# Kernel tuning notes

Measured on AMD Instinct MI355X. Metric: run time of the kernel, lower is better.

Reference implementation:

```python
import jax, jax.numpy as jnp
import numpy as np

UNITS = 4096        # output channels
IN_DIM = 4096       # row_count
LEVELS = 16         # codebook entries per output channel (4-bit)
GROUP = 128         # group_size
NGROUPS = (IN_DIM + GROUP - 1) // GROUP  # 32
BATCH = 16


def setup_inputs() -> dict:
    key = jax.random.key(0)
    k1, k2, k3, k4, k5, k6 = jax.random.split(key, 6)
    inputs = jax.random.normal(k1, (BATCH, IN_DIM), dtype=jnp.float32)
    codebooks = jax.random.normal(k2, (UNITS, LEVELS), dtype=jnp.float32)
    scales = jax.random.uniform(k3, (UNITS, NGROUPS), dtype=jnp.float32)
    residual = jax.random.normal(k4, (UNITS, NGROUPS, GROUP), dtype=jnp.float32) * 0.01
    bias = jax.random.normal(k5, (UNITS,), dtype=jnp.float32)
    indices = jax.random.randint(k6, (UNITS, NGROUPS, GROUP), 0, LEVELS, dtype=jnp.int32)
    return {"inputs": inputs, "codebooks": codebooks, "scales": scales,
            "residual": residual, "bias": bias, "indices": indices}


def _dequantize_kernel(codebooks, scales, residual, indices):
    oc, ng, gs = indices.shape
    # gathered[o, g, k] = codebooks[o, indices[o, g, k]]   (batch_dims=1 gather)
    gathered = jnp.take_along_axis(codebooks, indices.reshape(oc, ng * gs), axis=1)
    gathered = gathered.reshape(oc, ng, gs)
    grouped = gathered * scales[:, :, None] + residual          # [OC, G, K]
    kernel = jnp.transpose(grouped, (1, 2, 0)).reshape(ng * gs, oc)  # [G*K, OC]
    return kernel[:IN_DIM, :]


def reference(inputs, codebooks, scales, residual, bias, indices):
    kernel = _dequantize_kernel(codebooks, scales, residual, indices)  # [IN_DIM, UNITS]
    out = inputs @ kernel + bias  # activation=None
    return out
```

## Files before the change

kernel.cpp:

```cpp
#include <hip/hip_runtime.h>

#define UNITS   4096
#define IN_DIM  4096
#define LEVELS  16
#define NGROUPS 32
#define BATCH   16

#define OTILE  16
#define KSPLIT 4
#define KSTEP  128
#define NIT    8
#define WB_S   136

typedef __attribute__((ext_vector_type(8))) short bf16x8;
typedef __attribute__((ext_vector_type(4))) float f32x4;

__device__ __forceinline__ unsigned f2bf(float f) {
    unsigned u = __float_as_uint(f);
    u += 0x7FFF + ((u >> 16) & 1);
    return u >> 16;
}

__device__ __forceinline__ void gload16(const void* g, void* l) {
    __builtin_amdgcn_global_load_lds(
        (const __attribute__((address_space(1))) void*)g,
        (__attribute__((address_space(3))) void*)l, 16, 0, 0);
}

#define ELEM4I(v, j) ((j)==0?(v).x:((j)==1?(v).y:((j)==2?(v).z:(v).w)))

__global__ void aconv_kernel(const float* __restrict__ inputs,
                             unsigned short* __restrict__ A_frag)
{
    const int slot = blockIdx.x * 256 + threadIdx.x;
    const int ks = slot >> 6, lane = slot & 63;
    const int m  = lane & 15;
    const int kk = ks * 32 + ((lane >> 4) << 3);
    const float4 a = *reinterpret_cast<const float4*>(&inputs[m * IN_DIM + kk]);
    const float4 b = *reinterpret_cast<const float4*>(&inputs[m * IN_DIM + kk + 4]);
    uint4 pk;
    pk.x = f2bf(a.x) | (f2bf(a.y) << 16);
    pk.y = f2bf(a.z) | (f2bf(a.w) << 16);
    pk.z = f2bf(b.x) | (f2bf(b.y) << 16);
    pk.w = f2bf(b.z) | (f2bf(b.w) << 16);
    *reinterpret_cast<uint4*>(&A_frag[(size_t)slot * 8]) = pk;
}

__global__ __launch_bounds__(256, 4)
void turbo_mfma2(const float* __restrict__ codebooks,
                 const float* __restrict__ scales,
                 const float* __restrict__ residual,
                 const float* __restrict__ bias,
                 const int*   __restrict__ indices,
                 const unsigned short* __restrict__ A_frag,
                 float* __restrict__ out)
{
    __shared__ int   Idx[2][OTILE * KSTEP];
    __shared__ float Res[2][OTILE * KSTEP];
    __shared__ __align__(16) unsigned short Wb[OTILE * WB_S];
    __shared__ float cb[OTILE * LEVELS];
    __shared__ float scs[OTILE][NIT];

    const int tid = threadIdx.x;
    const int w   = tid >> 6, l = tid & 63;

    const int bx  = blockIdx.x;
    const int bxs = (bx & 7) * 128 + (bx >> 3);
    const int ot  = bxs >> 2;
    const int kq  = bxs & 3;
    const int obase   = ot * OTILE;
    const int kslice0 = kq * (NIT * KSTEP);

    cb[tid] = codebooks[obase * LEVELS + tid];
    if (tid < OTILE * NIT)
        scs[tid >> 3][tid & 7] =
            scales[(obase + (tid >> 3)) * NGROUPS + kq * NIT + (tid & 7)];

    uint4 aA[NIT];
    #pragma unroll
    for (int it = 0; it < NIT; ++it) {
        const int ksg = (kslice0 >> 5) + it * 4 + w;
        aA[it] = *reinterpret_cast<const uint4*>(&A_frag[((size_t)ksg * 64 + l) * 8]);
    }

#define STAGE(BUF, IT)                                                         \
    {                                                                          \
        const int kb_ = kslice0 + (IT) * KSTEP;                                \
        _Pragma("unroll")                                                      \
        for (int j = 0; j < 2; ++j) {                                          \
            const int c_ = w * 2 + j;                                          \
            const int o_ = 2 * c_ + (l >> 5);                                  \
            const size_t goff_ = (size_t)(obase + o_) * IN_DIM + kb_ + (l & 31) * 4; \
            gload16(&indices[goff_],  &Idx[BUF][c_ * 256]);                    \
            gload16(&residual[goff_], &Res[BUF][c_ * 256]);                    \
        }                                                                      \
    }

    STAGE(0, 0)
    __syncthreads();

    f32x4 acc = {0.f, 0.f, 0.f, 0.f};

    #pragma unroll
    for (int it = 0; it < NIT; ++it) {
        const int cur = it & 1;
        if (it + 1 < NIT) STAGE(cur ^ 1, it + 1)

        {
            const int base = tid * 4;
            const int4   i0 = *reinterpret_cast<const int4*>(&Idx[cur][base]);
            const int4   i1 = *reinterpret_cast<const int4*>(&Idx[cur][base + 1024]);
            const float4 r0 = *reinterpret_cast<const float4*>(&Res[cur][base]);
            const float4 r1 = *reinterpret_cast<const float4*>(&Res[cur][base + 1024]);
            const int o0 = tid >> 5, o1 = o0 + 8;
            const float s0 = scs[o0][it], s1 = scs[o1][it];
            const float* c0 = &cb[o0 * LEVELS];
            const float* c1 = &cb[o1 * LEVELS];
            const int k0 = (tid & 31) * 4;
            const unsigned q00 = f2bf(fmaf(c0[i0.x], s0, r0.x)) | (f2bf(fmaf(c0[i0.y], s0, r0.y)) << 16);
            const unsigned q01 = f2bf(fmaf(c0[i0.z], s0, r0.z)) | (f2bf(fmaf(c0[i0.w], s0, r0.w)) << 16);
            const unsigned q10 = f2bf(fmaf(c1[i1.x], s1, r1.x)) | (f2bf(fmaf(c1[i1.y], s1, r1.y)) << 16);
            const unsigned q11 = f2bf(fmaf(c1[i1.z], s1, r1.z)) | (f2bf(fmaf(c1[i1.w], s1, r1.w)) << 16);
            *reinterpret_cast<uint2*>(&Wb[o0 * WB_S + k0]) = make_uint2(q00, q01);
            *reinterpret_cast<uint2*>(&Wb[o1 * WB_S + k0]) = make_uint2(q10, q11);
        }
        __syncthreads();

        {
            const bf16x8 b = *reinterpret_cast<const bf16x8*>(
                &Wb[(l & 15) * WB_S + w * 32 + ((l >> 4) << 3)]);
            acc = __builtin_amdgcn_mfma_f32_16x16x32_bf16(
                *reinterpret_cast<const bf16x8*>(&aA[it]), b, acc, 0, 0, 0);
        }
        __syncthreads();
    }
#undef STAGE

    float* red = reinterpret_cast<float*>(Wb);
    if (w > 0)
        *reinterpret_cast<f32x4*>(&red[((w - 1) * 64 + l) * 4]) = acc;
    __syncthreads();
    if (w == 0) {
        #pragma unroll
        for (int v = 0; v < 3; ++v)
            acc += *reinterpret_cast<const f32x4*>(&red[(v * 64 + l) * 4]);
        const int col = obase + (l & 15);
        const float bv = (kq == 0) ? bias[col] : 0.f;
        #pragma unroll
        for (int q = 0; q < 4; ++q) {
            const int m = ((l >> 4) << 2) + q;
            atomicAdd(&out[m * UNITS + col], acc[q] + bv);
        }
    }
}

__global__ __launch_bounds__(256, 4)
void fallback_kernel(const float* __restrict__ inputs,
                     const float* __restrict__ codebooks,
                     const float* __restrict__ scales,
                     const float* __restrict__ residual,
                     const float* __restrict__ bias,
                     const int*   __restrict__ indices,
                     float* __restrict__ out)
{
    __shared__ float cb[16 * LEVELS];
    const int tid = threadIdx.x;
    const int ub = blockIdx.x & 255, ks = blockIdx.x >> 8;
    const int o_block = ub * 16;
    cb[tid] = codebooks[o_block * LEVELS + tid];
    __syncthreads();
    const int wave = tid >> 6, lane = tid & 63;
    const int o0 = o_block + wave * 4;
    const int k = ks * 256 + lane * 4;
    const int g = k >> 7;
    int4 idx[4]; float4 r[4]; float s[4];
    #pragma unroll
    for (int u = 0; u < 4; ++u) {
        const size_t off = (size_t)(o0 + u) * IN_DIM + k;
        idx[u] = *reinterpret_cast<const int4*>(&indices[off]);
        r[u]   = *reinterpret_cast<const float4*>(&residual[off]);
        s[u]   = scales[(o0 + u) * NGROUPS + g];
    }
    const float* cbw = &cb[wave * 4 * LEVELS];
    float wv[4][4];
    #pragma unroll
    for (int u = 0; u < 4; ++u) {
        wv[u][0] = fmaf(cbw[u * LEVELS + idx[u].x], s[u], r[u].x);
        wv[u][1] = fmaf(cbw[u * LEVELS + idx[u].y], s[u], r[u].y);
        wv[u][2] = fmaf(cbw[u * LEVELS + idx[u].z], s[u], r[u].z);
        wv[u][3] = fmaf(cbw[u * LEVELS + idx[u].w], s[u], r[u].w);
    }
    float acc[64];
    #pragma unroll
    for (int b = 0; b < BATCH; ++b) {
        const float4 in4 = *reinterpret_cast<const float4*>(&inputs[b * IN_DIM + k]);
        #pragma unroll
        for (int u = 0; u < 4; ++u) {
            float a = in4.x * wv[u][0];
            a = fmaf(in4.y, wv[u][1], a);
            a = fmaf(in4.z, wv[u][2], a);
            a = fmaf(in4.w, wv[u][3], a);
            acc[b * 4 + u] = a;
        }
    }
#define FOLD(S, N)                                         \
    {                                                      \
        const bool hi = (lane & (S)) != 0;                 \
        _Pragma("unroll")                                  \
        for (int t = 0; t < (N) / 2; ++t) {                \
            float a  = acc[2 * t];                         \
            float b2 = acc[2 * t + 1];                     \
            float send = hi ? a : b2;                      \
            float recv = __shfl_xor(send, (S));            \
            acc[t] = (hi ? b2 : a) + recv;                 \
        }                                                  \
    }
    FOLD(1, 64) FOLD(2, 32) FOLD(4, 16) FOLD(8, 8) FOLD(16, 4) FOLD(32, 2)
#undef FOLD
    const int b_ = lane >> 2, u_ = lane & 3;
    float v = acc[0];
    if (ks == 0) v += bias[o0 + u_];
    atomicAdd(&out[b_ * UNITS + o0 + u_], v);
}

extern "C" void kernel_launch(void* const* d_in, const int* in_sizes, int n_in,
                              void* d_out, int out_size, void* d_ws, size_t ws_size,
                              hipStream_t stream)
{
    const float* inputs    = (const float*)d_in[0];
    const float* codebooks = (const float*)d_in[1];
    const float* scales    = (const float*)d_in[2];
    const float* residual  = (const float*)d_in[3];
    const float* bias      = (const float*)d_in[4];
    const int*   indices   = (const int*)d_in[5];
    float* out = (float*)d_out;

    hipMemsetAsync(d_out, 0, (size_t)out_size * sizeof(float), stream);

    const size_t need = (size_t)128 * 64 * 8 * sizeof(unsigned short);
    if (ws_size >= need) {
        unsigned short* A_frag = (unsigned short*)d_ws;
        aconv_kernel<<<32, 256, 0, stream>>>(inputs, A_frag);
        turbo_mfma2<<<256 * KSPLIT, 256, 0, stream>>>(
            codebooks, scales, residual, bias, indices, A_frag, out);
    } else {
        fallback_kernel<<<256 * 16, 256, 0, stream>>>(
            inputs, codebooks, scales, residual, bias, indices, out);
    }
}
```

Before: 32.74 us.

## Deepen async LDS prefetch to two stages with explicit vmcnt waits

Restructures the double-buffered global-to-LDS pipeline so two stages are in flight: stage 0 is issued before the codebook, scale and A-fragment loads, and stage 1 right after the first barrier. Each iteration issues the load for it+2 into the buffer just consumed, and uses s_waitcnt vmcnt(4) plus a raw s_barrier instead of __syncthreads, so it waits only for the older stage. This aims to hide more HBM latency on the memory-bound indices and residual stream. The cost is fragile hand-written waitcnt accounting: the vmcnt(4) count assumes exactly four async loads per stage, and any other outstanding vector memory op would break it.

```diff
diff --git a/kernel.cpp b/kernel.cpp
--- a/kernel.cpp
+++ b/kernel.cpp
@@ -26,8 +26,6 @@
         (const __attribute__((address_space(1))) void*)g,
         (__attribute__((address_space(3))) void*)l, 16, 0, 0);
 }
-
-#define ELEM4I(v, j) ((j)==0?(v).x:((j)==1?(v).y:((j)==2?(v).z:(v).w)))
 
 __global__ void aconv_kernel(const float* __restrict__ inputs,
                              unsigned short* __restrict__ A_frag)
@@ -47,7 +45,7 @@
 }
 
 __global__ __launch_bounds__(256, 4)
-void turbo_mfma2(const float* __restrict__ codebooks,
+void turbo_mfma3(const float* __restrict__ codebooks,
                  const float* __restrict__ scales,
                  const float* __restrict__ residual,
                  const float* __restrict__ bias,
@@ -70,18 +68,6 @@
     const int kq  = bxs & 3;
     const int obase   = ot * OTILE;
     const int kslice0 = kq * (NIT * KSTEP);
-
-    cb[tid] = codebooks[obase * LEVELS + tid];
-    if (tid < OTILE * NIT)
-        scs[tid >> 3][tid & 7] =
-            scales[(obase + (tid >> 3)) * NGROUPS + kq * NIT + (tid & 7)];
-
-    uint4 aA[NIT];
-    #pragma unroll
-    for (int it = 0; it < NIT; ++it) {
-        const int ksg = (kslice0 >> 5) + it * 4 + w;
-        aA[it] = *reinterpret_cast<const uint4*>(&A_frag[((size_t)ksg * 64 + l) * 8]);
-    }
 
 #define STAGE(BUF, IT)                                                         \
     {                                                                          \
@@ -97,21 +83,36 @@
     }
 
     STAGE(0, 0)
-    __syncthreads();
+
+    cb[tid] = codebooks[obase * LEVELS + tid];
+    if (tid < OTILE * NIT)
+        scs[tid >> 3][tid & 7] =
+            scales[(obase + (tid >> 3)) * NGROUPS + kq * NIT + (tid & 7)];
+
+    uint4 aA[NIT];
+    #pragma unroll
+    for (int it = 0; it < NIT; ++it) {
+        const int ksg = (kslice0 >> 5) + it * 4 + w;
+        aA[it] = *reinterpret_cast<const uint4*>(&A_frag[((size_t)ksg * 64 + l) * 8]);
+    }
+
+    asm volatile("s_waitcnt vmcnt(0) lgkmcnt(0)" ::: "memory");
+    __builtin_amdgcn_s_barrier();
+
+    STAGE(1, 1)
 
     f32x4 acc = {0.f, 0.f, 0.f, 0.f};
 
     #pragma unroll
     for (int it = 0; it < NIT; ++it) {
-        const int cur = it & 1;
-        if (it + 1 < NIT) STAGE(cur ^ 1, it + 1)
+        const int b = it & 1;
 
         {
             const int base = tid * 4;
-            const int4   i0 = *reinterpret_cast<const int4*>(&Idx[cur][base]);
-            const int4   i1 = *reinterpret_cast<const int4*>(&Idx[cur][base + 1024]);
-            const float4 r0 = *reinterpret_cast<const float4*>(&Res[cur][base]);
-            const float4 r1 = *reinterpret_cast<const float4*>(&Res[cur][base + 1024]);
+            const int4   i0 = *reinterpret_cast<const int4*>(&Idx[b][base]);
+            const int4   i1 = *reinterpret_cast<const int4*>(&Idx[b][base + 1024]);
+            const float4 r0 = *reinterpret_cast<const float4*>(&Res[b][base]);
+            const float4 r1 = *reinterpret_cast<const float4*>(&Res[b][base + 1024]);
             const int o0 = tid >> 5, o1 = o0 + 8;
             const float s0 = scs[o0][it], s1 = scs[o1][it];
             const float* c0 = &cb[o0 * LEVELS];
@@ -124,18 +125,29 @@
             *reinterpret_cast<uint2*>(&Wb[o0 * WB_S + k0]) = make_uint2(q00, q01);
             *reinterpret_cast<uint2*>(&Wb[o1 * WB_S + k0]) = make_uint2(q10, q11);
         }
-        __syncthreads();
+        asm volatile("s_waitcnt lgkmcnt(0)" ::: "memory");
+        __builtin_amdgcn_s_barrier();
+
+        if (it + 2 < NIT) { STAGE(b, it + 2) }
 
         {
-            const bf16x8 b = *reinterpret_cast<const bf16x8*>(
+            const bf16x8 bfr = *reinterpret_cast<const bf16x8*>(
                 &Wb[(l & 15) * WB_S + w * 32 + ((l >> 4) << 3)]);
             acc = __builtin_amdgcn_mfma_f32_16x16x32_bf16(
-                *reinterpret_cast<const bf16x8*>(&aA[it]), b, acc, 0, 0, 0);
-        }
-        __syncthreads();
+                *reinterpret_cast<const bf16x8*>(&aA[it]), bfr, acc, 0, 0, 0);
+        }
+
+        if (it + 2 < NIT) {
+            asm volatile("s_waitcnt vmcnt(4)" ::: "memory");
+            __builtin_amdgcn_s_barrier();
+        } else if (it + 1 < NIT) {
+            asm volatile("s_waitcnt vmcnt(0)" ::: "memory");
+            __builtin_amdgcn_s_barrier();
+        }
     }
 #undef STAGE
 
+    __syncthreads();
     float* red = reinterpret_cast<float*>(Wb);
     if (w > 0)
         *reinterpret_cast<f32x4*>(&red[((w - 1) * 64 + l) * 4]) = acc;
@@ -241,7 +253,7 @@
     if (ws_size >= need) {
         unsigned short* A_frag = (unsigned short*)d_ws;
         aconv_kernel<<<32, 256, 0, stream>>>(inputs, A_frag);
-        turbo_mfma2<<<256 * KSPLIT, 256, 0, stream>>>(
+        turbo_mfma3<<<256 * KSPLIT, 256, 0, stream>>>(
             codebooks, scales, residual, bias, indices, A_frag, out);
     } else {
         fallback_kernel<<<256 * 16, 256, 0, stream>>>(
```

Result: slower. 33.43 us (+2.1%).
